# Optimization experiments

Hardware: AMD Instinct MI355X
Metric: run time of the kernel (lower is better)

## Reference

```python
import jax, jax.numpy as jnp
import numpy as np

EPS = 1e-8  # torch F.cosine_similarity norm clamp
TEMPERATURE = 0.05


def setup_inputs() -> dict:
    key = jax.random.key(0)
    k1, k2 = jax.random.split(key)
    N, D = 8192, 768
    query_embeddings = jax.random.normal(k1, (N, D), dtype=jnp.float32)
    content_embeddings = jax.random.normal(k2, (N, D), dtype=jnp.float32)
    return {"query_embeddings": query_embeddings, "content_embeddings": content_embeddings}


def reference(query_embeddings, content_embeddings):
    # cosine_similarity(q[:,None], c[None,:], dim=2) == normalize(q) @ normalize(c).T
    qn = query_embeddings / jnp.maximum(
        jnp.linalg.norm(query_embeddings, axis=-1, keepdims=True), EPS)
    cn = content_embeddings / jnp.maximum(
        jnp.linalg.norm(content_embeddings, axis=-1, keepdims=True), EPS)
    sim = jnp.einsum('nd,md->nm', qn, cn) / TEMPERATURE  # [N, N]
    # cross-entropy with targets = arange(N): positive is the diagonal
    logz = jax.nn.logsumexp(sim, axis=-1)                # [N]
    loss = jnp.mean(logz - jnp.diagonal(sim))
    return loss
```

## Files before the change

kernel.cpp:

```cpp
#include <hip/hip_runtime.h>
#include <hip/hip_bf16.h>


#define NROWS 8192
#define DDIM  768
#define ROWB  1536
#define NKT  (DDIM / 64)
#define NIT  (NKT / 2)
#define GRID_T (NROWS / 256)

constexpr float INV_TEMP = 20.0f;
constexpr float NORM_EPS = 1e-8f;

using bf16 = __hip_bfloat16;
typedef __attribute__((ext_vector_type(4))) float  f32x4;
typedef __attribute__((ext_vector_type(8))) short  bf16x8;

__global__ void norm_diag_kernel(const float* __restrict__ q, const float* __restrict__ c,
                                 bf16* __restrict__ qn, bf16* __restrict__ cn,
                                 float* __restrict__ diag) {
    const int row  = (blockIdx.x * 256 + threadIdx.x) >> 6;
    const int lane = threadIdx.x & 63;
    const float4* qv = (const float4*)(q + (size_t)row * DDIM);
    const float4* cv = (const float4*)(c + (size_t)row * DDIM);
    float4 a[3], b[3];
    #pragma unroll
    for (int j = 0; j < 3; ++j) { a[j] = qv[lane + j * 64]; b[j] = cv[lane + j * 64]; }
    float ssq = 0.f, ssc = 0.f, dot = 0.f;
    #pragma unroll
    for (int j = 0; j < 3; ++j) {
        ssq += a[j].x * a[j].x + a[j].y * a[j].y + a[j].z * a[j].z + a[j].w * a[j].w;
        ssc += b[j].x * b[j].x + b[j].y * b[j].y + b[j].z * b[j].z + b[j].w * b[j].w;
        dot += a[j].x * b[j].x + a[j].y * b[j].y + a[j].z * b[j].z + a[j].w * b[j].w;
    }
    #pragma unroll
    for (int m = 32; m; m >>= 1) {
        ssq += __shfl_xor(ssq, m);
        ssc += __shfl_xor(ssc, m);
        dot += __shfl_xor(dot, m);
    }
    float invq = 1.0f / fmaxf(sqrtf(ssq), NORM_EPS);
    float invc = 1.0f / fmaxf(sqrtf(ssc), NORM_EPS);
    if (lane == 0) diag[row] = dot * invq * invc * INV_TEMP;
    ushort4* qo = (ushort4*)(qn + (size_t)row * DDIM);
    ushort4* co = (ushort4*)(cn + (size_t)row * DDIM);
    #pragma unroll
    for (int j = 0; j < 3; ++j) {
        union { ushort4 u; bf16 h[4]; } oq, oc;
        oq.h[0] = __float2bfloat16(a[j].x * invq); oq.h[1] = __float2bfloat16(a[j].y * invq);
        oq.h[2] = __float2bfloat16(a[j].z * invq); oq.h[3] = __float2bfloat16(a[j].w * invq);
        oc.h[0] = __float2bfloat16(b[j].x * invc); oc.h[1] = __float2bfloat16(b[j].y * invc);
        oc.h[2] = __float2bfloat16(b[j].z * invc); oc.h[3] = __float2bfloat16(b[j].w * invc);
        qo[lane + j * 64] = oq.u;
        co[lane + j * 64] = oc.u;
    }
}

__device__ __forceinline__ void async16(void* l, const void* g) {
    __builtin_amdgcn_global_load_lds(
        (const __attribute__((address_space(1))) void*)g,
        (__attribute__((address_space(3))) void*)l, 16, 0, 0);
}

#define BARRIER __builtin_amdgcn_s_barrier()
#define SCHED0  __builtin_amdgcn_sched_barrier(0)
#define PRIO1   __builtin_amdgcn_s_setprio(1)
#define PRIO0   __builtin_amdgcn_s_setprio(0)
#define VMCNT(n) do { asm volatile("s_waitcnt vmcnt(" #n ")" ::: "memory"); } while (0)

#define STAGE_A(P, H, KT) do {                                              \
    const char* _g = aG + (size_t)(H) * 128 * ROWB + (size_t)(KT) * 128;    \
    char* _l = lds + (P) * 65536 + (H) * 16384 + dstW;                      \
    async16(_l, _g);                                                        \
    async16(_l + 8192, _g + 64 * ROWB);                                     \
} while (0)
#define STAGE_B(P, H, KT) do {                                              \
    const char* _g = bG + (size_t)(H) * 128 * ROWB + (size_t)(KT) * 128;    \
    char* _l = lds + 32768 + (P) * 65536 + (H) * 16384 + dstW;              \
    async16(_l, _g);                                                        \
    async16(_l + 8192, _g + 64 * ROWB);                                     \
} while (0)

#define READ_A(P, MH) do {                                                  \
    const char* _ab = lds + (P) * 65536 + aBaseT + (MH) * 64 * 128;         \
    _Pragma("unroll") for (int mi = 0; mi < 4; ++mi) {                      \
        a[mi][0] = *(const bf16x8*)(_ab + mi * 2048 + xk0);                 \
        a[mi][1] = *(const bf16x8*)(_ab + mi * 2048 + xk1);                 \
    }                                                                       \
} while (0)
#define READ_B(P, NH) do {                                                  \
    const char* _bb = lds + 32768 + (P) * 65536 + bBaseT + (NH) * 32 * 128; \
    _Pragma("unroll") for (int ni = 0; ni < 2; ++ni) {                      \
        bfr[NH][ni][0] = *(const bf16x8*)(_bb + ni * 2048 + xk0);           \
        bfr[NH][ni][1] = *(const bf16x8*)(_bb + ni * 2048 + xk1);           \
    }                                                                       \
} while (0)

#define MFMA_Q(MH, NH)                                                      \
    _Pragma("unroll") for (int mi = 0; mi < 4; ++mi)                        \
    _Pragma("unroll") for (int ni = 0; ni < 2; ++ni) {                      \
        acc[(MH)*4+mi][(NH)*2+ni] = __builtin_amdgcn_mfma_f32_16x16x32_bf16(\
            a[mi][0], bfr[NH][ni][0], acc[(MH)*4+mi][(NH)*2+ni], 0, 0, 0);  \
        acc[(MH)*4+mi][(NH)*2+ni] = __builtin_amdgcn_mfma_f32_16x16x32_bf16(\
            a[mi][1], bfr[NH][ni][1], acc[(MH)*4+mi][(NH)*2+ni], 0, 0, 0);  \
    }

__launch_bounds__(512, 2)
__global__ void simgemm_kernel(const bf16* __restrict__ A, const bf16* __restrict__ B,
                               float* __restrict__ partial) {
    __shared__ __attribute__((aligned(16))) char smem[131072];
    char* lds = smem;

    const int bid = blockIdx.x;
    const int tm = bid >> 5, tn = bid & 31;
    const int rowBase = tm * 256, colBase = tn * 256;
    const int tid = threadIdx.x;
    const int wid = tid >> 6, lane = tid & 63;
    const int wr = wid >> 2, wc = wid & 3;

    const int sr  = tid >> 3;
    const int scb = ((tid & 7) * 16) ^ ((sr & 7) << 4);
    const char* aG = (const char*)A + (size_t)(rowBase + sr) * ROWB + scb;
    const char* bG = (const char*)B + (size_t)(colBase + sr) * ROWB + scb;
    const int dstW = wid * 1024;

    const int aBaseT = wr * 16384 + (lane & 15) * 128;
    const int bBaseT = (wc >> 1) * 16384 + ((wc & 1) * 64 + (lane & 15)) * 128;
    const int klane  = (lane >> 4) * 16;
    const int swzr   = (lane & 7) << 4;
    const int xk0    = klane ^ swzr;
    const int xk1    = (64 + klane) ^ swzr;

    f32x4  acc[8][4] = {};
    bf16x8 a[4][2];
    bf16x8 bfr[2][2][2];

    STAGE_A(0, 0, 0); STAGE_A(0, 1, 0);
    STAGE_B(0, 0, 0); STAGE_B(0, 1, 0);
    STAGE_A(1, 0, 1); STAGE_A(1, 1, 1);
    VMCNT(4);
    BARRIER; SCHED0;
    READ_B(0, 0); READ_A(0, 0);
    SCHED0;

    #pragma unroll 1
    for (int i = 0; i < NIT; ++i) {
        const int t1 = 2 * i + 1;
        const int t2 = 2 * i + 2, t3 = 2 * i + 3;
        const bool more = (i + 1 < NIT);
        STAGE_B(1, 0, t1); STAGE_B(1, 1, t1);
        READ_B(0, 1); SCHED0;
        PRIO1; MFMA_Q(0, 0); MFMA_Q(0, 1); PRIO0;
        BARRIER; SCHED0;
        READ_A(0, 1); SCHED0;
        if (more) { STAGE_A(0, 0, t2); STAGE_A(0, 1, t2); }
        PRIO1; MFMA_Q(1, 0); MFMA_Q(1, 1); PRIO0;
        if (more) { VMCNT(4); } else { VMCNT(0); }
        BARRIER; SCHED0;
        READ_B(1, 0); READ_A(1, 0); SCHED0;
        if (more) { STAGE_B(0, 0, t2); STAGE_B(0, 1, t2); }
        READ_B(1, 1); SCHED0;
        PRIO1; MFMA_Q(0, 0); MFMA_Q(0, 1); PRIO0;
        BARRIER; SCHED0;
        READ_A(1, 1); SCHED0;
        if (more) { STAGE_A(1, 0, t3); STAGE_A(1, 1, t3); }
        PRIO1; MFMA_Q(1, 0); MFMA_Q(1, 1); PRIO0;
        if (more) { VMCNT(4); }
        BARRIER; SCHED0;
        if (more) { READ_B(0, 0); READ_A(0, 0); SCHED0; }
    }

    __syncthreads();
    float* red = (float*)smem;
    #pragma unroll
    for (int m = 0; m < 8; ++m) {
        #pragma unroll
        for (int r = 0; r < 4; ++r) {
            float s = 0.f;
            #pragma unroll
            for (int n = 0; n < 4; ++n)
                s += __expf(fmaf(INV_TEMP, acc[m][n][r], -INV_TEMP));
            s += __shfl_xor(s, 1);
            s += __shfl_xor(s, 2);
            s += __shfl_xor(s, 4);
            s += __shfl_xor(s, 8);
            if ((lane & 15) == 0)
                red[(wr * 128 + m * 16 + (lane >> 4) * 4 + r) * 4 + wc] = s;
        }
    }
    __syncthreads();
    if (tid < 256)
        partial[(size_t)(rowBase + tid) * GRID_T + tn] =
            red[tid * 4 + 0] + red[tid * 4 + 1] + red[tid * 4 + 2] + red[tid * 4 + 3];
}

__global__ void finalize_kernel(const float* __restrict__ partial,
                                const float* __restrict__ diag,
                                float* __restrict__ out) {
    int row = blockIdx.x * 256 + threadIdx.x;
    const float4* p = (const float4*)(partial + (size_t)row * GRID_T);
    float z = 0.f;
    #pragma unroll
    for (int i = 0; i < GRID_T / 4; ++i) {
        float4 v = p[i];
        z += v.x + v.y + v.z + v.w;
    }
    float term = INV_TEMP + logf(z) - diag[row];
    #pragma unroll
    for (int m = 32; m; m >>= 1) term += __shfl_xor(term, m);
    __shared__ float wsum[4];
    if ((threadIdx.x & 63) == 0) wsum[threadIdx.x >> 6] = term;
    __syncthreads();
    if (threadIdx.x == 0) {
        float s = wsum[0] + wsum[1] + wsum[2] + wsum[3];
        atomicAdd(out, s * (1.0f / NROWS));
    }
}

extern "C" void kernel_launch(void* const* d_in, const int* in_sizes, int n_in,
                              void* d_out, int out_size, void* d_ws, size_t ws_size,
                              hipStream_t stream) {
    const float* q = (const float*)d_in[0];
    const float* c = (const float*)d_in[1];
    float* out = (float*)d_out;

    char* ws = (char*)d_ws;
    bf16* qn = (bf16*)ws;
    bf16* cn = (bf16*)(ws + (size_t)NROWS * DDIM * 2);
    float* diag = (float*)(ws + (size_t)NROWS * DDIM * 4);
    float* partial = diag + NROWS;

    hipMemsetAsync(d_out, 0, sizeof(float), stream);

    norm_diag_kernel<<<NROWS / 4, 256, 0, stream>>>(q, c, qn, cn, diag);
    simgemm_kernel<<<GRID_T * GRID_T, 512, 0, stream>>>(qn, cn, partial);
    finalize_kernel<<<NROWS / 256, 256, 0, stream>>>(partial, diag, out);
}
```

Measured before the change: 192.2 us.

## Quantize normalized embeddings to FP8 and use scaled f8f6f4 MFMA

The normalization kernel now writes the unit-norm rows as packed FP8 (e4m3) instead of bf16, which halves the operand bytes. The similarity GEMM uses the 16x16x128 scaled f8f6f4 MFMA with unit scales. The LDS staging, swizzle and software pipeline are restructured around 128-byte K tiles, giving 6 k-steps instead of 12 bf16 tiles. The aim is to double matrix throughput per instruction and cut memory traffic, at the cost of lower precision in logits scaled by 20, which may hurt accuracy of the loss.

```diff
diff --git a/kernel.cpp b/kernel.cpp
--- a/kernel.cpp
+++ b/kernel.cpp
@@ -4,20 +4,18 @@
 
 #define NROWS 8192
 #define DDIM  768
-#define ROWB  1536
-#define NKT  (DDIM / 64)
-#define NIT  (NKT / 2)
+#define ROWB  768
+#define NKT   6
 #define GRID_T (NROWS / 256)
 
 constexpr float INV_TEMP = 20.0f;
 constexpr float NORM_EPS = 1e-8f;
 
-using bf16 = __hip_bfloat16;
 typedef __attribute__((ext_vector_type(4))) float  f32x4;
-typedef __attribute__((ext_vector_type(8))) short  bf16x8;
+typedef __attribute__((ext_vector_type(4))) int    i32x4;
 
 __global__ void norm_diag_kernel(const float* __restrict__ q, const float* __restrict__ c,
-                                 bf16* __restrict__ qn, bf16* __restrict__ cn,
+                                 char* __restrict__ qn, char* __restrict__ cn,
                                  float* __restrict__ diag) {
     const int row  = (blockIdx.x * 256 + threadIdx.x) >> 6;
     const int lane = threadIdx.x & 63;
@@ -42,17 +40,16 @@
     float invq = 1.0f / fmaxf(sqrtf(ssq), NORM_EPS);
     float invc = 1.0f / fmaxf(sqrtf(ssc), NORM_EPS);
     if (lane == 0) diag[row] = dot * invq * invc * INV_TEMP;
-    ushort4* qo = (ushort4*)(qn + (size_t)row * DDIM);
-    ushort4* co = (ushort4*)(cn + (size_t)row * DDIM);
+    int* qo = (int*)(qn + (size_t)row * ROWB);
+    int* co = (int*)(cn + (size_t)row * ROWB);
     #pragma unroll
     for (int j = 0; j < 3; ++j) {
-        union { ushort4 u; bf16 h[4]; } oq, oc;
-        oq.h[0] = __float2bfloat16(a[j].x * invq); oq.h[1] = __float2bfloat16(a[j].y * invq);
-        oq.h[2] = __float2bfloat16(a[j].z * invq); oq.h[3] = __float2bfloat16(a[j].w * invq);
-        oc.h[0] = __float2bfloat16(b[j].x * invc); oc.h[1] = __float2bfloat16(b[j].y * invc);
-        oc.h[2] = __float2bfloat16(b[j].z * invc); oc.h[3] = __float2bfloat16(b[j].w * invc);
-        qo[lane + j * 64] = oq.u;
-        co[lane + j * 64] = oc.u;
+        int wq = __builtin_amdgcn_cvt_pk_fp8_f32(a[j].x * invq, a[j].y * invq, 0, false);
+        wq     = __builtin_amdgcn_cvt_pk_fp8_f32(a[j].z * invq, a[j].w * invq, wq, true);
+        int wc = __builtin_amdgcn_cvt_pk_fp8_f32(b[j].x * invc, b[j].y * invc, 0, false);
+        wc     = __builtin_amdgcn_cvt_pk_fp8_f32(b[j].z * invc, b[j].w * invc, wc, true);
+        qo[lane + j * 64] = wq;
+        co[lane + j * 64] = wc;
     }
 }
 
@@ -68,45 +65,46 @@
 #define PRIO0   __builtin_amdgcn_s_setprio(0)
 #define VMCNT(n) do { asm volatile("s_waitcnt vmcnt(" #n ")" ::: "memory"); } while (0)
 
-#define STAGE_A(P, H, KT) do {                                              \
-    const char* _g = aG + (size_t)(H) * 128 * ROWB + (size_t)(KT) * 128;    \
-    char* _l = lds + (P) * 65536 + (H) * 16384 + dstW;                      \
+#define STAGE_A2(P, Q, KT) do {                                             \
+    const char* _g = aG + (size_t)(Q) * 64 * ROWB + (size_t)(KT) * 128;     \
+    char* _l = lds + (P) * 65536 + (Q) * 8192 + dstW;                       \
     async16(_l, _g);                                                        \
     async16(_l + 8192, _g + 64 * ROWB);                                     \
 } while (0)
-#define STAGE_B(P, H, KT) do {                                              \
-    const char* _g = bG + (size_t)(H) * 128 * ROWB + (size_t)(KT) * 128;    \
-    char* _l = lds + 32768 + (P) * 65536 + (H) * 16384 + dstW;              \
+#define STAGE_B2(P, Q, KT) do {                                             \
+    const char* _g = bG + (size_t)(Q) * 64 * ROWB + (size_t)(KT) * 128;     \
+    char* _l = lds + 32768 + (P) * 65536 + (Q) * 8192 + dstW;               \
     async16(_l, _g);                                                        \
     async16(_l + 8192, _g + 64 * ROWB);                                     \
 } while (0)
 
 #define READ_A(P, MH) do {                                                  \
-    const char* _ab = lds + (P) * 65536 + aBaseT + (MH) * 64 * 128;         \
+    const char* _ab = lds + (P) * 65536 + aBaseT + (MH) * 8192;             \
     _Pragma("unroll") for (int mi = 0; mi < 4; ++mi) {                      \
-        a[mi][0] = *(const bf16x8*)(_ab + mi * 2048 + xk0);                 \
-        a[mi][1] = *(const bf16x8*)(_ab + mi * 2048 + xk1);                 \
+        a[mi][0] = *(const i32x4*)(_ab + mi * 2048 + xk0);                  \
+        a[mi][1] = *(const i32x4*)(_ab + mi * 2048 + xk1);                  \
     }                                                                       \
 } while (0)
 #define READ_B(P, NH) do {                                                  \
-    const char* _bb = lds + 32768 + (P) * 65536 + bBaseT + (NH) * 32 * 128; \
+    const char* _bb = lds + 32768 + (P) * 65536 + bBaseT + (NH) * 4096;     \
     _Pragma("unroll") for (int ni = 0; ni < 2; ++ni) {                      \
-        bfr[NH][ni][0] = *(const bf16x8*)(_bb + ni * 2048 + xk0);           \
-        bfr[NH][ni][1] = *(const bf16x8*)(_bb + ni * 2048 + xk1);           \
+        bfr[NH][ni][0] = *(const i32x4*)(_bb + ni * 2048 + xk0);            \
+        bfr[NH][ni][1] = *(const i32x4*)(_bb + ni * 2048 + xk1);            \
     }                                                                       \
 } while (0)
 
-#define MFMA_Q(MH, NH)                                                      \
-    _Pragma("unroll") for (int mi = 0; mi < 4; ++mi)                        \
-    _Pragma("unroll") for (int ni = 0; ni < 2; ++ni) {                      \
-        acc[(MH)*4+mi][(NH)*2+ni] = __builtin_amdgcn_mfma_f32_16x16x32_bf16(\
-            a[mi][0], bfr[NH][ni][0], acc[(MH)*4+mi][(NH)*2+ni], 0, 0, 0);  \
-        acc[(MH)*4+mi][(NH)*2+ni] = __builtin_amdgcn_mfma_f32_16x16x32_bf16(\
-            a[mi][1], bfr[NH][ni][1], acc[(MH)*4+mi][(NH)*2+ni], 0, 0, 0);  \
-    }
+#define MFMA_Q(MH, NH)                                                        \
+    _Pragma("unroll") for (int mi = 0; mi < 4; ++mi)                          \
+    _Pragma("unroll") for (int ni = 0; ni < 2; ++ni)                          \
+        acc[(MH)*4+mi][(NH)*2+ni] =                                           \
+            __builtin_amdgcn_mfma_scale_f32_16x16x128_f8f6f4(                 \
+                __builtin_shufflevector(a[mi][0], a[mi][1], 0,1,2,3,4,5,6,7), \
+                __builtin_shufflevector(bfr[NH][ni][0], bfr[NH][ni][1],       \
+                                        0,1,2,3,4,5,6,7),                     \
+                acc[(MH)*4+mi][(NH)*2+ni], 0, 0, 0, 0x7F7F7F7F, 0, 0x7F7F7F7F);
 
 __launch_bounds__(512, 2)
-__global__ void simgemm_kernel(const bf16* __restrict__ A, const bf16* __restrict__ B,
+__global__ void simgemm_kernel(const char* __restrict__ A, const char* __restrict__ B,
                                float* __restrict__ partial) {
     __shared__ __attribute__((aligned(16))) char smem[131072];
     char* lds = smem;
@@ -120,54 +118,47 @@
 
     const int sr  = tid >> 3;
     const int scb = ((tid & 7) * 16) ^ ((sr & 7) << 4);
-    const char* aG = (const char*)A + (size_t)(rowBase + sr) * ROWB + scb;
-    const char* bG = (const char*)B + (size_t)(colBase + sr) * ROWB + scb;
+    const char* aG = A + (size_t)(rowBase + sr) * ROWB + scb;
+    const char* bG = B + (size_t)(colBase + sr) * ROWB + scb;
     const int dstW = wid * 1024;
 
-    const int aBaseT = wr * 16384 + (lane & 15) * 128;
-    const int bBaseT = (wc >> 1) * 16384 + ((wc & 1) * 64 + (lane & 15)) * 128;
-    const int klane  = (lane >> 4) * 16;
-    const int swzr   = (lane & 7) << 4;
-    const int xk0    = klane ^ swzr;
-    const int xk1    = (64 + klane) ^ swzr;
-
-    f32x4  acc[8][4] = {};
-    bf16x8 a[4][2];
-    bf16x8 bfr[2][2][2];
-
-    STAGE_A(0, 0, 0); STAGE_A(0, 1, 0);
-    STAGE_B(0, 0, 0); STAGE_B(0, 1, 0);
-    STAGE_A(1, 0, 1); STAGE_A(1, 1, 1);
-    VMCNT(4);
+    const int aBaseT = (wr * 128 + (lane & 15)) * 128;
+    const int bBaseT = (wc * 64 + (lane & 15)) * 128;
+    const int xk0    = ((lane >> 4) * 32) ^ ((lane & 7) << 4);
+    const int xk1    = xk0 ^ 16;
+
+    f32x4 acc[8][4] = {};
+    i32x4 a[4][2];
+    i32x4 bfr[2][2][2];
+
+    STAGE_A2(0, 0, 0); STAGE_A2(0, 2, 0);
+    STAGE_B2(0, 0, 0); STAGE_B2(0, 2, 0);
+    STAGE_A2(1, 0, 1);
+    VMCNT(2);
     BARRIER; SCHED0;
-    READ_B(0, 0); READ_A(0, 0);
+    READ_A(0, 0); READ_B(0, 0);
     SCHED0;
 
     #pragma unroll 1
-    for (int i = 0; i < NIT; ++i) {
-        const int t1 = 2 * i + 1;
-        const int t2 = 2 * i + 2, t3 = 2 * i + 3;
-        const bool more = (i + 1 < NIT);
-        STAGE_B(1, 0, t1); STAGE_B(1, 1, t1);
-        READ_B(0, 1); SCHED0;
-        PRIO1; MFMA_Q(0, 0); MFMA_Q(0, 1); PRIO0;
-        BARRIER; SCHED0;
-        READ_A(0, 1); SCHED0;
-        if (more) { STAGE_A(0, 0, t2); STAGE_A(0, 1, t2); }
-        PRIO1; MFMA_Q(1, 0); MFMA_Q(1, 1); PRIO0;
-        if (more) { VMCNT(4); } else { VMCNT(0); }
-        BARRIER; SCHED0;
-        READ_B(1, 0); READ_A(1, 0); SCHED0;
-        if (more) { STAGE_B(0, 0, t2); STAGE_B(0, 1, t2); }
-        READ_B(1, 1); SCHED0;
-        PRIO1; MFMA_Q(0, 0); MFMA_Q(0, 1); PRIO0;
-        BARRIER; SCHED0;
-        READ_A(1, 1); SCHED0;
-        if (more) { STAGE_A(1, 0, t3); STAGE_A(1, 1, t3); }
-        PRIO1; MFMA_Q(1, 0); MFMA_Q(1, 1); PRIO0;
-        if (more) { VMCNT(4); }
-        BARRIER; SCHED0;
-        if (more) { READ_B(0, 0); READ_A(0, 0); SCHED0; }
+    for (int i = 0; i < NKT; ++i) {
+        const int P = i & 1;
+        const int t1 = i + 1, t2 = i + 2;
+        if (t1 < NKT) STAGE_A2(P ^ 1, 2, t1);
+        PRIO1; MFMA_Q(0, 0); PRIO0;
+        BARRIER; SCHED0;
+        READ_B(P, 1); SCHED0;
+        if (t1 < NKT) STAGE_B2(P ^ 1, 0, t1);
+        PRIO1; MFMA_Q(0, 1); PRIO0;
+        BARRIER; SCHED0;
+        READ_A(P, 1); SCHED0;
+        if (t1 < NKT) STAGE_B2(P ^ 1, 2, t1);
+        PRIO1; MFMA_Q(1, 0); PRIO0;
+        BARRIER; SCHED0;
+        if (t2 < NKT) STAGE_A2(P, 0, t2);
+        PRIO1; MFMA_Q(1, 1); PRIO0;
+        if (t2 < NKT) { VMCNT(2); } else { VMCNT(0); }
+        BARRIER; SCHED0;
+        if (t1 < NKT) { READ_A(P ^ 1, 0); READ_B(P ^ 1, 0); SCHED0; }
     }
 
     __syncthreads();
@@ -225,9 +216,9 @@
     float* out = (float*)d_out;
 
     char* ws = (char*)d_ws;
-    bf16* qn = (bf16*)ws;
-    bf16* cn = (bf16*)(ws + (size_t)NROWS * DDIM * 2);
-    float* diag = (float*)(ws + (size_t)NROWS * DDIM * 4);
+    char* qn = ws;
+    char* cn = ws + (size_t)NROWS * ROWB;
+    float* diag = (float*)(ws + (size_t)2 * NROWS * ROWB);
     float* partial = diag + NROWS;
 
     hipMemsetAsync(d_out, 0, sizeof(float), stream);
```

Result: slower. 222.8 us (+15.9%).
